# Kernel tuning notes

Hardware: AMD Instinct MI355X
Metric: run time of the kernel (lower is better)

## Reference

```python
import jax, jax.numpy as jnp
import numpy as np
from jax import lax

N = 2_097_152  # grid length
WENO5_MULT_BIAS = 0.1


def _conv1d(x, w, b, pad):
    # x: [1, C_in, L], w: [C_out, C_in, K] -> [1, C_out, L]
    y = lax.conv_general_dilated(x, w, window_strides=(1,), padding=[(pad, pad)],
                                 dimension_numbers=('NCH', 'OIH', 'NCH'))
    return y + b[None, :, None]


def _inner_nn_weno5(dif, w1, b1, w2, b2, w3, b3, w4, b4, w5, b5, w6, b6):
    # dif: [N] -> multiplier signal [N] in (0,1) via sigmoid
    x = dif[None, None, :]
    x = jax.nn.elu(_conv1d(x, w1, b1, 2))
    x = jax.nn.elu(_conv1d(x, w2, b2, 2))
    x = jax.nn.elu(_conv1d(x, w3, b3, 0))
    x = jax.nn.elu(_conv1d(x, w4, b4, 0))
    x = jax.nn.elu(_conv1d(x, w5, b5, 1))
    x = jax.nn.sigmoid(_conv1d(x, w6, b6, 0))
    return x[0, 0, :]


def _avg_diff(uu):
    # centered average of forward differences, replicated at the edges -> [N]
    dif = uu[1:] - uu[:-1]
    dif_left = jnp.concatenate([dif, dif[-1:]])
    dif_right = jnp.concatenate([dif[:1], dif])
    return 0.5 * dif_left + 0.5 * dif_right


def _fluxes_minus(u):
    f0 = (11 * u[3:-2] - 7 * u[4:-1] + 2 * u[5:]) / 6
    f1 = (2 * u[2:-3] + 5 * u[3:-2] - u[4:-1]) / 6
    f2 = (-u[1:-4] + 5 * u[2:-3] + 2 * u[3:-2]) / 6
    return f0, f1, f2


def _betas_minus(u):
    b0 = 13 / 12 * (u[3:-2] - 2 * u[4:-1] + u[5:]) ** 2 + 1 / 4 * (3 * u[3:-2] - 4 * u[4:-1] + u[5:]) ** 2
    b1 = 13 / 12 * (u[2:-3] - 2 * u[3:-2] + u[4:-1]) ** 2 + 1 / 4 * (u[2:-3] - u[4:-1]) ** 2
    b2 = 13 / 12 * (u[1:-4] - 2 * u[2:-3] + u[3:-2]) ** 2 + 1 / 4 * (u[1:-4] - 4 * u[2:-3] + 3 * u[3:-2]) ** 2
    return b0, b1, b2


def _weno5(uu, e, beta_mult):
    # w5_minus=True, mweno=True, mapped=False, trainable=True branch
    ur = uu[1:]
    ul = uu[:-1]
    fp = _fluxes_minus(ur)
    fn = _fluxes_minus(ul)
    bp = _betas_minus(ur)
    bn = _betas_minus(ul)
    # multipliers bm[3+shift:-3+shift] for shift in {-1,0,1}
    mul = (beta_mult[2:-4], beta_mult[3:-3], beta_mult[4:-2])
    bp = [b * m for b, m in zip(bp, mul)]
    bn = [b * m for b, m in zip(bn, mul)]
    ds = (1 / 10, 6 / 10, 3 / 10)

    def omegas_mweno(bs):
        brs = (bs[2] - bs[0]) ** 2
        o = [d / (e + b) ** 2 * (brs + (e + b) ** 2) for b, d in zip(bs, ds)]
        s = o[0] + o[1] + o[2]
        return [x / s for x in o]

    op = omegas_mweno(bp)
    on = omegas_mweno(bn)
    fluxp = op[0] * fp[0] + op[1] * fp[1] + op[2] * fp[2]
    fluxn = on[0] * fn[0] + on[1] * fn[1] + on[2] * fn[2]
    return fluxp - fluxn  # [N-6]


def setup_inputs() -> dict:
    key = jax.random.key(0)
    ks = jax.random.split(key, 14)
    uu = jax.random.normal(ks[0], (N,), dtype=jnp.float32)
    e = jnp.float32(1e-6)
    s = 0.1  # weight scale for stability
    w1 = s * jax.random.normal(ks[1], (20, 1, 5), jnp.float32)
    b1 = s * jax.random.normal(ks[2], (20,), jnp.float32)
    w2 = s * jax.random.normal(ks[3], (40, 20, 5), jnp.float32)
    b2 = s * jax.random.normal(ks[4], (40,), jnp.float32)
    w3 = s * jax.random.normal(ks[5], (80, 40, 1), jnp.float32)
    b3 = s * jax.random.normal(ks[6], (80,), jnp.float32)
    w4 = s * jax.random.normal(ks[7], (40, 80, 1), jnp.float32)
    b4 = s * jax.random.normal(ks[8], (40,), jnp.float32)
    w5 = s * jax.random.normal(ks[9], (20, 40, 3), jnp.float32)
    b5 = s * jax.random.normal(ks[10], (20,), jnp.float32)
    w6 = s * jax.random.normal(ks[11], (1, 20, 1), jnp.float32)
    b6 = s * jax.random.normal(ks[12], (1,), jnp.float32)
    return {"uu": uu, "e": e, "w1": w1, "b1": b1, "w2": w2, "b2": b2,
            "w3": w3, "b3": b3, "w4": w4, "b4": b4, "w5": w5, "b5": b5,
            "w6": w6, "b6": b6}


def reference(uu, e, w1, b1, w2, b2, w3, b3, w4, b4, w5, b5, w6, b6):
    dif = _avg_diff(uu)
    beta_mult = _inner_nn_weno5(dif, w1, b1, w2, b2, w3, b3, w4, b4, w5, b5, w6, b6) + WENO5_MULT_BIAS
    return _weno5(uu, e, beta_mult)
```

## Files before the change

### kernel.cpp

```cpp
#include <hip/hip_runtime.h>
#include <math.h>

#define NTHREADS 256
#define TOUT 126
#define NP 128
#define X1ROWS 132
#define X1S 40
#define X2S 40
#define T3S 80
#define X4S 40
#define X5S 26
#define NDIF 136
#define NUU 138

#define F2_BASE 0
#define F3_BASE 15
#define F4_BASE 25
#define F5_BASE 34
#define NFRAGS 42

typedef unsigned short u16;
typedef unsigned int u32;
typedef __attribute__((ext_vector_type(8))) short bf16x8;
typedef __attribute__((ext_vector_type(4))) float f32x4;

__device__ __forceinline__ float elu_f(float x) {
    return x > 0.0f ? x : (__expf(x) - 1.0f);
}
__device__ __forceinline__ float sq_f(float x) { return x * x; }
__device__ __forceinline__ u16 f2bf(float f) {
    union { float f; u32 u; } v; v.f = f;
    u32 r = v.u + 0x7FFFu + ((v.u >> 16) & 1u);
    return (u16)(r >> 16);
}
__device__ __forceinline__ float bf2f(u16 h) {
    union { u32 u; float f; } v; v.u = ((u32)h) << 16;
    return v.f;
}
__device__ __forceinline__ u32 pack_trunc(float a, float b) {
    union { float f; u32 u; } va, vb; va.f = a; vb.f = b;
#if __has_builtin(__builtin_amdgcn_perm)
    return __builtin_amdgcn_perm(vb.u, va.u, 0x07060302u);
#else
    return (vb.u & 0xFFFF0000u) | (va.u >> 16);
#endif
}

__global__ __launch_bounds__(64) void build_frags_kernel(
    const float* __restrict__ w2, const float* __restrict__ w3,
    const float* __restrict__ w4, const float* __restrict__ w5,
    u16* __restrict__ ws)
{
    const int f = blockIdx.x;
    const int lane = threadIdx.x;
    const int m = lane & 15;
    const int q = lane >> 4;
    float wvv[8];
    #pragma unroll
    for (int j = 0; j < 8; ++j) wvv[j] = 0.0f;

    if (f < F3_BASE) {
        int mt = (f - F2_BASE) / 5, s = (f - F2_BASE) % 5;
        int oc = mt * 16 + m;
        #pragma unroll
        for (int j = 0; j < 8; ++j) {
            int ic = q * 8 + j;
            if (oc < 40 && ic < 20) wvv[j] = w2[oc * 100 + ic * 5 + s];
        }
    } else if (f < F4_BASE) {
        int mt = (f - F3_BASE) / 2, s = (f - F3_BASE) % 2;
        int oc = mt * 16 + m;
        #pragma unroll
        for (int j = 0; j < 8; ++j) {
            int k = s * 32 + q * 8 + j;
            if (k < 40) wvv[j] = w3[oc * 40 + k];
        }
    } else if (f < F5_BASE) {
        int mt = (f - F4_BASE) / 3, s = (f - F4_BASE) % 3;
        int oc = mt * 16 + m;
        #pragma unroll
        for (int j = 0; j < 8; ++j) {
            int k = s * 32 + q * 8 + j;
            if (oc < 40 && k < 80) wvv[j] = w4[oc * 80 + k];
        }
    } else {
        int mt = (f - F5_BASE) / 4, s = (f - F5_BASE) % 4;
        int oc = mt * 16 + m;
        int k0 = s * 32 + q * 8;
        int dk = k0 / 40, ic0 = k0 - dk * 40;
        #pragma unroll
        for (int j = 0; j < 8; ++j) {
            if (oc < 20 && k0 < 120) wvv[j] = w5[oc * 120 + (ic0 + j) * 3 + dk];
        }
    }
    u32 pk[4];
    #pragma unroll
    for (int p = 0; p < 4; ++p)
        pk[p] = (u32)f2bf(wvv[2 * p]) | ((u32)f2bf(wvv[2 * p + 1]) << 16);
    u32* wp = (u32*)&ws[(f * 64 + lane) * 8];
    wp[0] = pk[0]; wp[1] = pk[1]; wp[2] = pk[2]; wp[3] = pk[3];
}

__device__ __forceinline__ bf16x8 ld_frag(const u16* ws, int f, int lane) {
    return *(const bf16x8*)&ws[(f * 64 + lane) * 8];
}

__global__ __launch_bounds__(NTHREADS, 5) void weno_nn_kernel(
    const float* __restrict__ uu, const float* __restrict__ e_ptr,
    const float* __restrict__ w1, const float* __restrict__ b1,
    const float* __restrict__ b2, const float* __restrict__ b3,
    const float* __restrict__ b4, const float* __restrict__ b5,
    const float* __restrict__ w6, const float* __restrict__ b6,
    const u16* __restrict__ wfr,
    float* __restrict__ out, int n_out, int N)
{
    __shared__ float s_uu[NUU];
    __shared__ float s_dif[NDIF];
    __shared__ __align__(16) u16 bufA[NP * T3S];
    __shared__ __align__(16) u16 bufB[130 * X4S];

    const int tid  = threadIdx.x;
    const int lane = tid & 63;
    const int wv_id = __builtin_amdgcn_readfirstlane(tid >> 6);
    const int m    = lane & 15;
    const int q    = lane >> 4;
    const int J0   = blockIdx.x * TOUT;
    const int P0   = J0 + 2;
    const int U0   = J0 - 4;

    for (int i = tid; i < NUU; i += NTHREADS) {
        int g = U0 + i;
        s_uu[i] = (g >= 0 && g < N) ? uu[g] : 0.0f;
    }
    __syncthreads();

    for (int d = tid; d < NDIF; d += NTHREADS) {
        int g = P0 - 5 + d;
        float v = 0.0f;
        if (g >= 0 && g < N) {
            int j1 = g < N - 2 ? g : N - 2;
            int j0 = g - 1 > 0 ? g - 1 : 0;
            float dl = s_uu[j1 + 1 - U0] - s_uu[j1 - U0];
            float dr = s_uu[j0 + 1 - U0] - s_uu[j0 - U0];
            v = 0.5f * (dl + dr);
        }
        s_dif[d] = v;
    }
    __syncthreads();

    for (int s = tid; s < X1ROWS; s += NTHREADS) {
        int g = P0 - 3 + s;
        bool valid = (g >= 0 && g < N);
        float dv[5];
        #pragma unroll
        for (int k = 0; k < 5; ++k) dv[k] = s_dif[s + k];
        float v[20];
        #pragma unroll
        for (int oc = 0; oc < 20; ++oc) {
            float a = b1[oc];
            #pragma unroll
            for (int k = 0; k < 5; ++k) a += w1[oc * 5 + k] * dv[k];
            v[oc] = valid ? elu_f(a) : 0.0f;
        }
        u32* rp = (u32*)&bufA[s * X1S];
        #pragma unroll
        for (int p = 0; p < 10; ++p)
            rp[p] = pack_trunc(v[2 * p], v[2 * p + 1]);
        #pragma unroll
        for (int p = 10; p < 16; ++p) rp[p] = 0;
    }
    __syncthreads();

    {
        bf16x8 a2[3][5];
        #pragma unroll
        for (int mt = 0; mt < 3; ++mt)
            #pragma unroll
            for (int s = 0; s < 5; ++s)
                a2[mt][s] = ld_frag(wfr, F2_BASE + mt * 5 + s, lane);
        f32x4 bias2[3];
        #pragma unroll
        for (int mt = 0; mt < 3; ++mt) {
            #pragma unroll
            for (int r = 0; r < 4; ++r) {
                int oc = mt * 16 + 4 * q + r;
                bias2[mt][r] = (oc < 40) ? b2[oc] : 0.0f;
            }
        }
        for (int t = 0; t < 2; ++t) {
            const int N0 = (wv_id * 2 + t) * 16;
            f32x4 acc[3];
            #pragma unroll
            for (int mt = 0; mt < 3; ++mt) acc[mt] = bias2[mt];
            #pragma unroll
            for (int s = 0; s < 5; ++s) {
                bf16x8 bfrag = *(const bf16x8*)&bufA[(N0 + m + s) * X1S + q * 8];
                #pragma unroll
                for (int mt = 0; mt < 3; ++mt)
                    acc[mt] = __builtin_amdgcn_mfma_f32_16x16x32_bf16(a2[mt][s], bfrag, acc[mt], 0, 0, 0);
            }
            #pragma unroll
            for (int mt = 0; mt < 3; ++mt) {
                int oc0 = mt * 16 + 4 * q;
                if (oc0 < 40) {
                    u32* wp = (u32*)&bufB[(N0 + m) * X2S + oc0];
                    wp[0] = pack_trunc(elu_f(acc[mt][0]), elu_f(acc[mt][1]));
                    wp[1] = pack_trunc(elu_f(acc[mt][2]), elu_f(acc[mt][3]));
                }
            }
        }
    }
    __syncthreads();

    {
        bf16x8 a3[5][2];
        #pragma unroll
        for (int mt = 0; mt < 5; ++mt)
            #pragma unroll
            for (int s = 0; s < 2; ++s)
                a3[mt][s] = ld_frag(wfr, F3_BASE + mt * 2 + s, lane);
        f32x4 bias3[5];
        #pragma unroll
        for (int mt = 0; mt < 5; ++mt) {
            #pragma unroll
            for (int r = 0; r < 4; ++r) bias3[mt][r] = b3[mt * 16 + 4 * q + r];
        }
        for (int t = 0; t < 2; ++t) {
            const int N0 = (wv_id * 2 + t) * 16;
            f32x4 acc[5];
            #pragma unroll
            for (int mt = 0; mt < 5; ++mt) acc[mt] = bias3[mt];
            {
                bf16x8 bfrag = *(const bf16x8*)&bufB[(N0 + m) * X2S + q * 8];
                #pragma unroll
                for (int mt = 0; mt < 5; ++mt)
                    acc[mt] = __builtin_amdgcn_mfma_f32_16x16x32_bf16(a3[mt][0], bfrag, acc[mt], 0, 0, 0);
            }
            {
                bf16x8 bfrag = *(const bf16x8*)&bufB[(N0 + m) * X2S + ((q == 0) ? 32 : 0)];
                #pragma unroll
                for (int mt = 0; mt < 5; ++mt)
                    acc[mt] = __builtin_amdgcn_mfma_f32_16x16x32_bf16(a3[mt][1], bfrag, acc[mt], 0, 0, 0);
            }
            #pragma unroll
            for (int mt = 0; mt < 5; ++mt) {
                int oc0 = mt * 16 + 4 * q;
                u32* wp = (u32*)&bufA[(N0 + m) * T3S + oc0];
                wp[0] = pack_trunc(elu_f(acc[mt][0]), elu_f(acc[mt][1]));
                wp[1] = pack_trunc(elu_f(acc[mt][2]), elu_f(acc[mt][3]));
            }
        }
    }
    __syncthreads();

    {
        bf16x8 a4[3][3];
        #pragma unroll
        for (int mt = 0; mt < 3; ++mt)
            #pragma unroll
            for (int s = 0; s < 3; ++s)
                a4[mt][s] = ld_frag(wfr, F4_BASE + mt * 3 + s, lane);
        f32x4 bias4[3];
        #pragma unroll
        for (int mt = 0; mt < 3; ++mt) {
            #pragma unroll
            for (int r = 0; r < 4; ++r) {
                int oc = mt * 16 + 4 * q + r;
                bias4[mt][r] = (oc < 40) ? b4[oc] : 0.0f;
            }
        }
        if (tid < 80) bufB[128 * X4S + tid] = 0;
        for (int t = 0; t < 2; ++t) {
            const int N0 = (wv_id * 2 + t) * 16;
            f32x4 acc[3];
            #pragma unroll
            for (int mt = 0; mt < 3; ++mt) acc[mt] = bias4[mt];
            #pragma unroll
            for (int s = 0; s < 3; ++s) {
                int k0 = s * 32 + q * 8;
                bf16x8 bfrag = *(const bf16x8*)&bufA[(N0 + m) * T3S + ((k0 < 80) ? k0 : 0)];
                #pragma unroll
                for (int mt = 0; mt < 3; ++mt)
                    acc[mt] = __builtin_amdgcn_mfma_f32_16x16x32_bf16(a4[mt][s], bfrag, acc[mt], 0, 0, 0);
            }
            #pragma unroll
            for (int mt = 0; mt < 3; ++mt) {
                int oc0 = mt * 16 + 4 * q;
                if (oc0 < 40) {
                    u32* wp = (u32*)&bufB[(N0 + m) * X4S + oc0];
                    wp[0] = pack_trunc(elu_f(acc[mt][0]), elu_f(acc[mt][1]));
                    wp[1] = pack_trunc(elu_f(acc[mt][2]), elu_f(acc[mt][3]));
                }
            }
        }
    }
    __syncthreads();

    {
        bf16x8 a5[2][4];
        #pragma unroll
        for (int mt = 0; mt < 2; ++mt)
            #pragma unroll
            for (int s = 0; s < 4; ++s)
                a5[mt][s] = ld_frag(wfr, F5_BASE + mt * 4 + s, lane);
        f32x4 bias5[2];
        #pragma unroll
        for (int mt = 0; mt < 2; ++mt) {
            #pragma unroll
            for (int r = 0; r < 4; ++r) {
                int oc = mt * 16 + 4 * q + r;
                bias5[mt][r] = (oc < 20) ? b5[oc] : 0.0f;
            }
        }
        for (int t = 0; t < 2; ++t) {
            const int N0 = (wv_id * 2 + t) * 16;
            f32x4 acc[2];
            #pragma unroll
            for (int mt = 0; mt < 2; ++mt) acc[mt] = bias5[mt];
            #pragma unroll
            for (int s = 0; s < 4; ++s) {
                int k0 = s * 32 + q * 8;
                int dk = (k0 < 120) ? (k0 / 40) : 0;
                int ic0 = (k0 < 120) ? (k0 - dk * 40) : 0;
                bf16x8 bfrag = *(const bf16x8*)&bufB[(N0 + m + dk) * X4S + ic0];
                #pragma unroll
                for (int mt = 0; mt < 2; ++mt)
                    acc[mt] = __builtin_amdgcn_mfma_f32_16x16x32_bf16(a5[mt][s], bfrag, acc[mt], 0, 0, 0);
            }
            #pragma unroll
            for (int mt = 0; mt < 2; ++mt) {
                int oc0 = mt * 16 + 4 * q;
                if (oc0 < 20) {
                    u32* wp = (u32*)&bufA[(N0 + m) * X5S + oc0];
                    wp[0] = pack_trunc(elu_f(acc[mt][0]), elu_f(acc[mt][1]));
                    wp[1] = pack_trunc(elu_f(acc[mt][2]), elu_f(acc[mt][3]));
                }
            }
        }
    }
    __syncthreads();

    if (tid < NP) {
        float a = b6[0];
        #pragma unroll
        for (int c = 0; c < 20; ++c)
            a += w6[c] * bf2f(bufA[tid * X5S + c]);
        s_dif[tid] = 1.0f / (1.0f + __expf(-a)) + 0.1f;
    }
    __syncthreads();

    const float eps = e_ptr[0];
    if (tid < TOUT) {
        int j = J0 + tid;
        if (j < n_out) {
            float a  = s_uu[tid + 5];
            float b  = s_uu[tid + 6];
            float c  = s_uu[tid + 7];
            float d  = s_uu[tid + 8];
            float ee = s_uu[tid + 9];
            float f  = s_uu[tid + 10];
            float m0 = s_dif[tid];
            float m1 = s_dif[tid + 1];
            float m2 = s_dif[tid + 2];

            const float i6 = 1.0f / 6.0f;
            float fp0 = (11.f * d - 7.f * ee + 2.f * f) * i6;
            float fp1 = (2.f * c + 5.f * d - ee) * i6;
            float fp2 = (-b + 5.f * c + 2.f * d) * i6;
            float fn0 = (11.f * c - 7.f * d + 2.f * ee) * i6;
            float fn1 = (2.f * b + 5.f * c - d) * i6;
            float fn2 = (-a + 5.f * b + 2.f * c) * i6;

            const float c1312 = 13.f / 12.f;
            float bp0 = c1312 * sq_f(d - 2.f * ee + f) + 0.25f * sq_f(3.f * d - 4.f * ee + f);
            float bp1 = c1312 * sq_f(c - 2.f * d + ee) + 0.25f * sq_f(c - ee);
            float bp2 = c1312 * sq_f(b - 2.f * c + d) + 0.25f * sq_f(b - 4.f * c + 3.f * d);
            float bn0 = c1312 * sq_f(c - 2.f * d + ee) + 0.25f * sq_f(3.f * c - 4.f * d + ee);
            float bn1 = c1312 * sq_f(b - 2.f * c + d) + 0.25f * sq_f(b - d);
            float bn2 = c1312 * sq_f(a - 2.f * b + c) + 0.25f * sq_f(a - 4.f * b + 3.f * c);

            bp0 *= m0; bp1 *= m1; bp2 *= m2;
            bn0 *= m0; bn1 *= m1; bn2 *= m2;

            float q0 = eps + bp0; q0 *= q0;
            float q1 = eps + bp1; q1 *= q1;
            float q2 = eps + bp2; q2 *= q2;
            float brs = bp2 - bp0; brs *= brs;
            float o0 = 0.1f * (1.f + brs / q0);
            float o1 = 0.6f * (1.f + brs / q1);
            float o2 = 0.3f * (1.f + brs / q2);
            float inv = 1.f / (o0 + o1 + o2);
            float fluxp = (o0 * fp0 + o1 * fp1 + o2 * fp2) * inv;

            q0 = eps + bn0; q0 *= q0;
            q1 = eps + bn1; q1 *= q1;
            q2 = eps + bn2; q2 *= q2;
            brs = bn2 - bn0; brs *= brs;
            o0 = 0.1f * (1.f + brs / q0);
            o1 = 0.6f * (1.f + brs / q1);
            o2 = 0.3f * (1.f + brs / q2);
            inv = 1.f / (o0 + o1 + o2);
            float fluxn = (o0 * fn0 + o1 * fn1 + o2 * fn2) * inv;

            out[j] = fluxp - fluxn;
        }
    }
}

extern "C" void kernel_launch(void* const* d_in, const int* in_sizes, int n_in,
                              void* d_out, int out_size, void* d_ws, size_t ws_size,
                              hipStream_t stream) {
    const float* uu = (const float*)d_in[0];
    const float* e  = (const float*)d_in[1];
    const float* w1 = (const float*)d_in[2];
    const float* b1 = (const float*)d_in[3];
    const float* w2 = (const float*)d_in[4];
    const float* b2 = (const float*)d_in[5];
    const float* w3 = (const float*)d_in[6];
    const float* b3 = (const float*)d_in[7];
    const float* w4 = (const float*)d_in[8];
    const float* b4 = (const float*)d_in[9];
    const float* w5 = (const float*)d_in[10];
    const float* b5 = (const float*)d_in[11];
    const float* w6 = (const float*)d_in[12];
    const float* b6 = (const float*)d_in[13];
    float* out = (float*)d_out;
    u16* wfr = (u16*)d_ws;
    const int N = in_sizes[0];
    const int nblocks = (out_size + TOUT - 1) / TOUT;

    build_frags_kernel<<<NFRAGS, 64, 0, stream>>>(w2, w3, w4, w5, wfr);
    weno_nn_kernel<<<nblocks, NTHREADS, 0, stream>>>(
        uu, e, w1, b1, b2, b3, b4, b5, w6, b6, wfr,
        out, out_size, N);
}
```

Baseline: 319.6 us.

## Move conv1 onto MFMA and prefetch next-layer weight fragments before barriers

Replaces the scalar per-row first convolution with a bf16 MFMA over fragments built from w1 in the prep kernel, with inputs rounded to bf16. Each layer's weight fragments and biases are now loaded before the preceding barrier so the global-load latency overlaps the current layer's MFMA work. Launch bounds drop from 5 to 2 waves per EU, which raises the register budget for the live fragments but may lower occupancy. It also pads the T3S stride, writes a branchless ELU, and swaps divisions for hardware reciprocals, which trades some precision.

```diff
diff --git a/kernel.cpp b/kernel.cpp
--- a/kernel.cpp
+++ b/kernel.cpp
@@ -7,17 +7,19 @@
 #define X1ROWS 132
 #define X1S 40
 #define X2S 40
-#define T3S 80
+#define T3S 88
 #define X4S 40
 #define X5S 26
 #define NDIF 136
+#define NDIFP 152
 #define NUU 138
 
 #define F2_BASE 0
 #define F3_BASE 15
 #define F4_BASE 25
 #define F5_BASE 34
-#define NFRAGS 42
+#define F1_BASE 42
+#define NFRAGS 44
 
 typedef unsigned short u16;
 typedef unsigned int u32;
@@ -25,7 +27,10 @@
 typedef __attribute__((ext_vector_type(4))) float f32x4;
 
 __device__ __forceinline__ float elu_f(float x) {
-    return x > 0.0f ? x : (__expf(x) - 1.0f);
+    return fmaxf(x, __expf(fminf(x, 0.0f)) - 1.0f);
+}
+__device__ __forceinline__ float rcp_f(float x) {
+    return __builtin_amdgcn_rcpf(x);
 }
 __device__ __forceinline__ float sq_f(float x) { return x * x; }
 __device__ __forceinline__ u16 f2bf(float f) {
@@ -45,11 +50,14 @@
     return (vb.u & 0xFFFF0000u) | (va.u >> 16);
 #endif
 }
+__device__ __forceinline__ u32 pack_rne(float a, float b) {
+    return (u32)f2bf(a) | ((u32)f2bf(b) << 16);
+}
 
 __global__ __launch_bounds__(64) void build_frags_kernel(
-    const float* __restrict__ w2, const float* __restrict__ w3,
-    const float* __restrict__ w4, const float* __restrict__ w5,
-    u16* __restrict__ ws)
+    const float* __restrict__ w1, const float* __restrict__ w2,
+    const float* __restrict__ w3, const float* __restrict__ w4,
+    const float* __restrict__ w5, u16* __restrict__ ws)
 {
     const int f = blockIdx.x;
     const int lane = threadIdx.x;
@@ -83,7 +91,7 @@
             int k = s * 32 + q * 8 + j;
             if (oc < 40 && k < 80) wvv[j] = w4[oc * 80 + k];
         }
-    } else {
+    } else if (f < F1_BASE) {
         int mt = (f - F5_BASE) / 4, s = (f - F5_BASE) % 4;
         int oc = mt * 16 + m;
         int k0 = s * 32 + q * 8;
@@ -91,6 +99,14 @@
         #pragma unroll
         for (int j = 0; j < 8; ++j) {
             if (oc < 20 && k0 < 120) wvv[j] = w5[oc * 120 + (ic0 + j) * 3 + dk];
+        }
+    } else {
+        int mt = f - F1_BASE;
+        int oc = mt * 16 + m;
+        #pragma unroll
+        for (int j = 0; j < 8; ++j) {
+            int k = q * 8 + j;
+            if (oc < 20 && k < 5) wvv[j] = w1[oc * 5 + k];
         }
     }
     u32 pk[4];
@@ -105,7 +121,7 @@
     return *(const bf16x8*)&ws[(f * 64 + lane) * 8];
 }
 
-__global__ __launch_bounds__(NTHREADS, 5) void weno_nn_kernel(
+__global__ __launch_bounds__(NTHREADS, 2) void weno_nn_kernel(
     const float* __restrict__ uu, const float* __restrict__ e_ptr,
     const float* __restrict__ w1, const float* __restrict__ b1,
     const float* __restrict__ b2, const float* __restrict__ b3,
@@ -115,7 +131,7 @@
     float* __restrict__ out, int n_out, int N)
 {
     __shared__ float s_uu[NUU];
-    __shared__ float s_dif[NDIF];
+    __shared__ float s_dif[NDIFP];
     __shared__ __align__(16) u16 bufA[NP * T3S];
     __shared__ __align__(16) u16 bufB[130 * X4S];
 
@@ -128,16 +144,31 @@
     const int P0   = J0 + 2;
     const int U0   = J0 - 4;
 
+    bf16x8 a1[2];     f32x4 bias1[2];
+    bf16x8 a2[3][5];  f32x4 bias2[3];
+    bf16x8 a3[5][2];  f32x4 bias3[5];
+    bf16x8 a4[3][3];  f32x4 bias4[3];
+    bf16x8 a5[2][4];  f32x4 bias5[2];
+
+    a1[0] = ld_frag(wfr, F1_BASE + 0, lane);
+    a1[1] = ld_frag(wfr, F1_BASE + 1, lane);
+    #pragma unroll
+    for (int r = 0; r < 4; ++r) {
+        bias1[0][r] = b1[4 * q + r];
+        int oc = 16 + 4 * q + r;
+        bias1[1][r] = (oc < 20) ? b1[oc] : 0.0f;
+    }
+
     for (int i = tid; i < NUU; i += NTHREADS) {
         int g = U0 + i;
         s_uu[i] = (g >= 0 && g < N) ? uu[g] : 0.0f;
     }
     __syncthreads();
 
-    for (int d = tid; d < NDIF; d += NTHREADS) {
+    for (int d = tid; d < NDIFP; d += NTHREADS) {
         int g = P0 - 5 + d;
         float v = 0.0f;
-        if (g >= 0 && g < N) {
+        if (d < NDIF && g >= 0 && g < N) {
             int j1 = g < N - 2 ? g : N - 2;
             int j0 = g - 1 > 0 ? g - 1 : 0;
             float dl = s_uu[j1 + 1 - U0] - s_uu[j1 - U0];
@@ -148,45 +179,66 @@
     }
     __syncthreads();
 
-    for (int s = tid; s < X1ROWS; s += NTHREADS) {
-        int g = P0 - 3 + s;
-        bool valid = (g >= 0 && g < N);
-        float dv[5];
-        #pragma unroll
-        for (int k = 0; k < 5; ++k) dv[k] = s_dif[s + k];
-        float v[20];
-        #pragma unroll
-        for (int oc = 0; oc < 20; ++oc) {
-            float a = b1[oc];
-            #pragma unroll
-            for (int k = 0; k < 5; ++k) a += w1[oc * 5 + k] * dv[k];
-            v[oc] = valid ? elu_f(a) : 0.0f;
-        }
-        u32* rp = (u32*)&bufA[s * X1S];
-        #pragma unroll
-        for (int p = 0; p < 10; ++p)
-            rp[p] = pack_trunc(v[2 * p], v[2 * p + 1]);
-        #pragma unroll
-        for (int p = 10; p < 16; ++p) rp[p] = 0;
-    }
-    __syncthreads();
-
     {
-        bf16x8 a2[3][5];
+        for (int idx = wv_id; idx < 9; idx += 4) {
+            const int N0 = idx * 16;
+            float d0 = s_dif[N0 + m + 0];
+            float d1 = s_dif[N0 + m + 1];
+            float d2 = s_dif[N0 + m + 2];
+            float d3 = s_dif[N0 + m + 3];
+            float d4 = s_dif[N0 + m + 4];
+            bf16x8 bfrag;
+            u32* bw = (u32*)&bfrag;
+            bw[0] = pack_rne(d0, d1);
+            bw[1] = pack_rne(d2, d3);
+            bw[2] = pack_rne(d4, 0.0f);
+            bw[3] = 0;
+            f32x4 acc0 = bias1[0];
+            f32x4 acc1 = bias1[1];
+            acc0 = __builtin_amdgcn_mfma_f32_16x16x32_bf16(a1[0], bfrag, acc0, 0, 0, 0);
+            acc1 = __builtin_amdgcn_mfma_f32_16x16x32_bf16(a1[1], bfrag, acc1, 0, 0, 0);
+            int pos = N0 + m;
+            if (pos < X1ROWS) {
+                int g = P0 - 3 + pos;
+                bool valid = (g >= 0 && g < N);
+                float e0 = valid ? elu_f(acc0[0]) : 0.0f;
+                float e1 = valid ? elu_f(acc0[1]) : 0.0f;
+                float e2 = valid ? elu_f(acc0[2]) : 0.0f;
+                float e3 = valid ? elu_f(acc0[3]) : 0.0f;
+                u32* wp = (u32*)&bufA[pos * X1S + 4 * q];
+                wp[0] = pack_trunc(e0, e1);
+                wp[1] = pack_trunc(e2, e3);
+                if (q == 0) {
+                    float f0 = valid ? elu_f(acc1[0]) : 0.0f;
+                    float f1 = valid ? elu_f(acc1[1]) : 0.0f;
+                    float f2 = valid ? elu_f(acc1[2]) : 0.0f;
+                    float f3 = valid ? elu_f(acc1[3]) : 0.0f;
+                    u32* wp2 = (u32*)&bufA[pos * X1S + 16];
+                    wp2[0] = pack_trunc(f0, f1);
+                    wp2[1] = pack_trunc(f2, f3);
+                }
+            }
+        }
+        for (int i2 = tid; i2 < X1ROWS * 6; i2 += NTHREADS) {
+            int rr = i2 / 6, cc = i2 - rr * 6;
+            *(u32*)&bufA[rr * X1S + 20 + 2 * cc] = 0;
+        }
         #pragma unroll
         for (int mt = 0; mt < 3; ++mt)
             #pragma unroll
             for (int s = 0; s < 5; ++s)
                 a2[mt][s] = ld_frag(wfr, F2_BASE + mt * 5 + s, lane);
-        f32x4 bias2[3];
-        #pragma unroll
-        for (int mt = 0; mt < 3; ++mt) {
+        #pragma unroll
+        for (int mt = 0; mt < 3; ++mt)
             #pragma unroll
             for (int r = 0; r < 4; ++r) {
                 int oc = mt * 16 + 4 * q + r;
                 bias2[mt][r] = (oc < 40) ? b2[oc] : 0.0f;
             }
-        }
+    }
+    __syncthreads();
+
+    {
         for (int t = 0; t < 2; ++t) {
             const int N0 = (wv_id * 2 + t) * 16;
             f32x4 acc[3];
@@ -209,22 +261,19 @@
                 }
             }
         }
-    }
-    __syncthreads();
-
-    {
-        bf16x8 a3[5][2];
         #pragma unroll
         for (int mt = 0; mt < 5; ++mt)
             #pragma unroll
             for (int s = 0; s < 2; ++s)
                 a3[mt][s] = ld_frag(wfr, F3_BASE + mt * 2 + s, lane);
-        f32x4 bias3[5];
-        #pragma unroll
-        for (int mt = 0; mt < 5; ++mt) {
+        #pragma unroll
+        for (int mt = 0; mt < 5; ++mt)
             #pragma unroll
             for (int r = 0; r < 4; ++r) bias3[mt][r] = b3[mt * 16 + 4 * q + r];
-        }
+    }
+    __syncthreads();
+
+    {
         for (int t = 0; t < 2; ++t) {
             const int N0 = (wv_id * 2 + t) * 16;
             f32x4 acc[5];
@@ -250,25 +299,22 @@
                 wp[1] = pack_trunc(elu_f(acc[mt][2]), elu_f(acc[mt][3]));
             }
         }
-    }
-    __syncthreads();
-
-    {
-        bf16x8 a4[3][3];
         #pragma unroll
         for (int mt = 0; mt < 3; ++mt)
             #pragma unroll
             for (int s = 0; s < 3; ++s)
                 a4[mt][s] = ld_frag(wfr, F4_BASE + mt * 3 + s, lane);
-        f32x4 bias4[3];
-        #pragma unroll
-        for (int mt = 0; mt < 3; ++mt) {
+        #pragma unroll
+        for (int mt = 0; mt < 3; ++mt)
             #pragma unroll
             for (int r = 0; r < 4; ++r) {
                 int oc = mt * 16 + 4 * q + r;
                 bias4[mt][r] = (oc < 40) ? b4[oc] : 0.0f;
             }
-        }
+    }
+    __syncthreads();
+
+    {
         if (tid < 80) bufB[128 * X4S + tid] = 0;
         for (int t = 0; t < 2; ++t) {
             const int N0 = (wv_id * 2 + t) * 16;
@@ -293,25 +339,22 @@
                 }
             }
         }
-    }
-    __syncthreads();
-
-    {
-        bf16x8 a5[2][4];
         #pragma unroll
         for (int mt = 0; mt < 2; ++mt)
             #pragma unroll
             for (int s = 0; s < 4; ++s)
                 a5[mt][s] = ld_frag(wfr, F5_BASE + mt * 4 + s, lane);
-        f32x4 bias5[2];
-        #pragma unroll
-        for (int mt = 0; mt < 2; ++mt) {
+        #pragma unroll
+        for (int mt = 0; mt < 2; ++mt)
             #pragma unroll
             for (int r = 0; r < 4; ++r) {
                 int oc = mt * 16 + 4 * q + r;
                 bias5[mt][r] = (oc < 20) ? b5[oc] : 0.0f;
             }
-        }
+    }
+    __syncthreads();
+
+    {
         for (int t = 0; t < 2; ++t) {
             const int N0 = (wv_id * 2 + t) * 16;
             f32x4 acc[2];
@@ -345,7 +388,7 @@
         #pragma unroll
         for (int c = 0; c < 20; ++c)
             a += w6[c] * bf2f(bufA[tid * X5S + c]);
-        s_dif[tid] = 1.0f / (1.0f + __expf(-a)) + 0.1f;
+        s_dif[tid] = rcp_f(1.0f + __expf(-a)) + 0.1f;
     }
     __syncthreads();
 
@@ -386,20 +429,20 @@
             float q1 = eps + bp1; q1 *= q1;
             float q2 = eps + bp2; q2 *= q2;
             float brs = bp2 - bp0; brs *= brs;
-            float o0 = 0.1f * (1.f + brs / q0);
-            float o1 = 0.6f * (1.f + brs / q1);
-            float o2 = 0.3f * (1.f + brs / q2);
-            float inv = 1.f / (o0 + o1 + o2);
+            float o0 = 0.1f * (1.f + brs * rcp_f(q0));
+            float o1 = 0.6f * (1.f + brs * rcp_f(q1));
+            float o2 = 0.3f * (1.f + brs * rcp_f(q2));
+            float inv = rcp_f(o0 + o1 + o2);
             float fluxp = (o0 * fp0 + o1 * fp1 + o2 * fp2) * inv;
 
             q0 = eps + bn0; q0 *= q0;
             q1 = eps + bn1; q1 *= q1;
             q2 = eps + bn2; q2 *= q2;
             brs = bn2 - bn0; brs *= brs;
-            o0 = 0.1f * (1.f + brs / q0);
-            o1 = 0.6f * (1.f + brs / q1);
-            o2 = 0.3f * (1.f + brs / q2);
-            inv = 1.f / (o0 + o1 + o2);
+            o0 = 0.1f * (1.f + brs * rcp_f(q0));
+            o1 = 0.6f * (1.f + brs * rcp_f(q1));
+            o2 = 0.3f * (1.f + brs * rcp_f(q2));
+            inv = rcp_f(o0 + o1 + o2);
             float fluxn = (o0 * fn0 + o1 * fn1 + o2 * fn2) * inv;
 
             out[j] = fluxp - fluxn;
@@ -429,7 +472,7 @@
     const int N = in_sizes[0];
     const int nblocks = (out_size + TOUT - 1) / TOUT;
 
-    build_frags_kernel<<<NFRAGS, 64, 0, stream>>>(w2, w3, w4, w5, wfr);
+    build_frags_kernel<<<NFRAGS, 64, 0, stream>>>(w1, w2, w3, w4, w5, wfr);
     weno_nn_kernel<<<nblocks, NTHREADS, 0, stream>>>(
         uu, e, w1, b1, b2, b3, b4, b5, w6, b6, wfr,
         out, out_size, N);
```

After: 259.8 us. -18.7%, faster.
